# Performance work log

Measured on AMD Instinct MI355X. Metric: run time of the kernel, lower is better.

Reference implementation:

```python
import jax, jax.numpy as jnp
import numpy as np

L, H, D, FF = 4, 16, 1024, 4   # nLayers, nHeads, embedDim, ffMult
EPS = 1e-5


def layernorm(x, g, b):
    mu = jnp.mean(x, axis=-1, keepdims=True)
    var = jnp.mean(jnp.square(x - mu), axis=-1, keepdims=True)
    return (x - mu) * jax.lax.rsqrt(var + EPS) * g + b


def setup_inputs() -> dict:
    key = jax.random.key(0)
    ks = jax.random.split(key, 4)
    B, N = 2, 2048
    s = 0.02
    return {
        "x": jax.random.normal(ks[0], (B, N, D), jnp.float32),
        "Wqkv": jax.random.normal(ks[1], (L, D, 3 * D), jnp.float32) * s,
        "bqkv": jnp.zeros((L, 3 * D), jnp.float32),
        "W1": jax.random.normal(ks[2], (L, D, FF * D), jnp.float32) * s,
        "b1": jnp.zeros((L, FF * D), jnp.float32),
        "W2": jax.random.normal(ks[3], (L, FF * D, D), jnp.float32) * s,
        "b2": jnp.zeros((L, D), jnp.float32),
        "g1": jnp.ones((L, D), jnp.float32),
        "be1": jnp.zeros((L, D), jnp.float32),
        "g2": jnp.ones((L, D), jnp.float32),
        "be2": jnp.zeros((L, D), jnp.float32),
    }


def reference(x, Wqkv, bqkv, W1, b1, W2, b2, g1, be1, g2, be2):
    B, N, _ = x.shape
    dh = D // H
    scale = D ** -0.5  # NOTE: module scales by embedDim**-0.5, not head_dim
    act = lambda t: jax.nn.gelu(t, approximate=False)
    for l in range(L):
        qkv = x @ Wqkv[l] + bqkv[l]                       # [B,N,3D]
        q, k, v = jnp.split(qkv, 3, axis=-1)
        q = q.reshape(B, N, H, dh)
        k = k.reshape(B, N, H, dh)
        v = v.reshape(B, N, H, dh)
        scores = jnp.einsum('bihd,bjhd->bhij', q, k) * scale  # [B,H,N,N]
        z = jax.nn.softmax(scores, axis=-1)
        o = jnp.einsum('bhij,bjhd->bihd', z, v).reshape(B, N, D)
        h = layernorm(o + x, g1[l], be1[l])               # post-LN residual 1
        f = act(h @ W1[l] + b1[l])
        f = act(f @ W2[l] + b2[l])                        # activation after 2nd linear too (as in Sequential)
        x = layernorm(f + h, g2[l], be2[l])               # post-LN residual 2
    return x
```

## Files before the change

kernel.cpp:

```cpp
#include <hip/hip_runtime.h>
#include <hip/hip_bf16.h>
#include <cmath>


typedef __attribute__((ext_vector_type(8))) short bf16x8;
typedef __attribute__((ext_vector_type(4))) float f32x4;
typedef __hip_bfloat16 bf16;

#define DEV static __device__ __forceinline__

DEV unsigned short f2b(float f) {
    bf16 h = __float2bfloat16(f);
    return *reinterpret_cast<unsigned short*>(&h);
}

DEV unsigned int pack_bf16(float lo, float hi) {
    return (unsigned int)f2b(lo) | ((unsigned int)f2b(hi) << 16);
}

DEV float b2f(unsigned short u) {
    unsigned int x = ((unsigned int)u) << 16;
    return *reinterpret_cast<float*>(&x);
}

DEV float gelu_fast(float x) {
    float u = 0.7978845608028654f * fmaf(0.044715f * x, x * x, x);
    u = fminf(fmaxf(u, -15.f), 15.f);
    float t = __builtin_amdgcn_exp2f(u * 2.8853900817779268f);
    float th = (t - 1.0f) * __builtin_amdgcn_rcpf(t + 1.0f);
    return 0.5f * x * (1.0f + th);
}

DEV void gload_lds16(const bf16* g, bf16* l) {
    __builtin_amdgcn_global_load_lds(
        (const __attribute__((address_space(1))) void*)g,
        (__attribute__((address_space(3))) void*)l, 16, 0, 0);
}

__global__ __launch_bounds__(256) void transpose_cast(const float* __restrict__ W,
                                                      bf16* __restrict__ Wt,
                                                      int K, int Nm) {
    __shared__ float tile[32][33];
    const int l = blockIdx.z;
    const float* Wl = W + (size_t)l * K * Nm;
    bf16* Wtl = Wt + (size_t)l * K * Nm;
    const int n0 = blockIdx.x * 32, k0 = blockIdx.y * 32;
    const int tx = threadIdx.x, ty = threadIdx.y;
#pragma unroll
    for (int i = 0; i < 4; ++i)
        tile[ty + 8 * i][tx] = Wl[(size_t)(k0 + ty + 8 * i) * Nm + n0 + tx];
    __syncthreads();
#pragma unroll
    for (int i = 0; i < 4; ++i)
        Wtl[(size_t)(n0 + ty + 8 * i) * K + k0 + tx] = __float2bfloat16(tile[tx][ty + 8 * i]);
}

__global__ __launch_bounds__(256) void vtrans(const bf16* __restrict__ qkv,
                                              bf16* __restrict__ vtg, int N) {
    __shared__ bf16 tile[32][33];
    const int bh = blockIdx.z, b = bh >> 4, h = bh & 15;
    const int n0 = blockIdx.x * 32, d0 = blockIdx.y * 32;
    const int tx = threadIdx.x, ty = threadIdx.y;
    const bf16* src = qkv + (size_t)(b * N + n0) * 3072 + 2048 + h * 64 + d0;
#pragma unroll
    for (int i = 0; i < 4; ++i)
        tile[ty + 8 * i][tx] = src[(size_t)(ty + 8 * i) * 3072 + tx];
    __syncthreads();
    bf16* dst = vtg + ((size_t)bh * 64 + d0) * N + n0;
#pragma unroll
    for (int i = 0; i < 4; ++i)
        dst[(size_t)(ty + 8 * i) * N + tx] = tile[tx][ty + 8 * i];
}

__global__ __launch_bounds__(256) void cast_bf16_k(const float* __restrict__ in,
                                                   bf16* __restrict__ out, int n4) {
    int i = blockIdx.x * 256 + threadIdx.x;
    if (i >= n4) return;
    float4 v = reinterpret_cast<const float4*>(in)[i];
    ushort4 o = { f2b(v.x), f2b(v.y), f2b(v.z), f2b(v.w) };
    reinterpret_cast<ushort4*>(out)[i] = o;
}

template <int EPI>
__global__ __launch_bounds__(512, 2) void gemm256(const bf16* __restrict__ A,
                                                  const bf16* __restrict__ Bt,
                                                  const float* __restrict__ bias,
                                                  void* __restrict__ Cout,
                                                  int M, int Nm, int K,
                                                  int nbx, int ntiles, int Ktotal) {
    __shared__ bf16 As[2][256][64];
    __shared__ bf16 Bs[2][256][64];
    const int nwg = gridDim.x;
    int id = blockIdx.x;
    id = (id & 7) * (nwg >> 3) + (id >> 3);
    const int tile = id % ntiles, split = id / ntiles;
    const int m0 = (tile / nbx) * 256, n0 = (tile % nbx) * 256;
    const int kbase = split * K;
    const int t = threadIdx.x, w = t >> 6, lane = t & 63;
    const int wm = w >> 2, wn = w & 3;
    const int lr = lane & 15, lg = lane >> 4;
    const int srow = w * 8;
    const bf16* Ag = A + (size_t)(m0 + srow + (lane >> 3)) * Ktotal + kbase + (lane & 7) * 8;
    const bf16* Bg = Bt + (size_t)(n0 + srow + (lane >> 3)) * Ktotal + kbase + (lane & 7) * 8;

    f32x4 acc[8][4] = {};
    const int NT = K / 64;

#define STAGE256(kt, b)                                                          \
    {                                                                            \
        const size_t koff = (size_t)(kt) * 64;                                   \
        _Pragma("unroll")                                                        \
        for (int p = 0; p < 4; ++p)                                              \
            gload_lds16(Ag + (size_t)(p * 64) * Ktotal + koff,                   \
                        &As[b][p * 64 + srow][0]);                               \
        _Pragma("unroll")                                                        \
        for (int p = 0; p < 4; ++p)                                              \
            gload_lds16(Bg + (size_t)(p * 64) * Ktotal + koff,                   \
                        &Bs[b][p * 64 + srow][0]);                               \
    }

    STAGE256(0, 0);
    for (int kt = 0; kt < NT; ++kt) {
        const int buf = kt & 1;
        if (kt + 1 < NT) {
            STAGE256(kt + 1, buf ^ 1);
            asm volatile("s_waitcnt vmcnt(8)" ::: "memory");
        } else {
            asm volatile("s_waitcnt vmcnt(0)" ::: "memory");
        }
        __builtin_amdgcn_sched_barrier(0);
        __builtin_amdgcn_s_barrier();
        __builtin_amdgcn_sched_barrier(0);
        __builtin_amdgcn_s_setprio(1);
#pragma unroll
        for (int kk = 0; kk < 2; ++kk) {
            const int lk = kk * 32 + lg * 8;
            bf16x8 a[8], b[4];
#pragma unroll
            for (int m = 0; m < 8; ++m)
                a[m] = *reinterpret_cast<const bf16x8*>(&As[buf][wm * 128 + m * 16 + lr][lk]);
#pragma unroll
            for (int n = 0; n < 4; ++n)
                b[n] = *reinterpret_cast<const bf16x8*>(&Bs[buf][wn * 64 + n * 16 + lr][lk]);
#pragma unroll
            for (int m = 0; m < 8; ++m)
#pragma unroll
                for (int n = 0; n < 4; ++n)
                    acc[m][n] = __builtin_amdgcn_mfma_f32_16x16x32_bf16(a[m], b[n], acc[m][n], 0, 0, 0);
        }
        __builtin_amdgcn_s_setprio(0);
        __builtin_amdgcn_sched_barrier(0);
        __builtin_amdgcn_s_barrier();
        __builtin_amdgcn_sched_barrier(0);
    }
#undef STAGE256

    if (EPI == 3) {
        bf16* outp = (bf16*)Cout + (size_t)split * M * Nm;
#pragma unroll
        for (int n = 0; n < 4; ++n) {
            const int col = n0 + wn * 64 + n * 16 + lr;
#pragma unroll
            for (int m = 0; m < 8; ++m) {
                const int row = m0 + wm * 128 + m * 16 + lg * 4;
#pragma unroll
                for (int j = 0; j < 4; ++j)
                    outp[(size_t)(row + j) * Nm + col] = __float2bfloat16(acc[m][n][j]);
            }
        }
    } else {
#pragma unroll
        for (int n = 0; n < 4; ++n) {
            const int col = n0 + wn * 64 + n * 16 + lr;
            const float bc = bias[col];
#pragma unroll
            for (int m = 0; m < 8; ++m) {
                const int row = m0 + wm * 128 + m * 16 + lg * 4;
#pragma unroll
                for (int j = 0; j < 4; ++j) {
                    float v = acc[m][n][j] + bc;
                    if (EPI == 1) v = gelu_fast(v);
                    reinterpret_cast<bf16*>(Cout)[(size_t)(row + j) * Nm + col] = __float2bfloat16(v);
                }
            }
        }
    }
}

__global__ __launch_bounds__(256) void reduce4_gelu(const bf16* __restrict__ part,
                                                    const float* __restrict__ bias,
                                                    float* __restrict__ out,
                                                    int n8, int Nm8, size_t stride) {
    int i = blockIdx.x * 256 + threadIdx.x;
    if (i >= n8) return;
    const int cb = (i % Nm8) * 8;
    float s[8];
#pragma unroll
    for (int e = 0; e < 8; ++e) s[e] = bias[cb + e];
#pragma unroll
    for (int k = 0; k < 4; ++k) {
        bf16x8 v = *reinterpret_cast<const bf16x8*>(part + (size_t)k * stride + (size_t)i * 8);
#pragma unroll
        for (int e = 0; e < 8; ++e) s[e] += b2f((unsigned short)v[e]);
    }
    float4 r0 = { gelu_fast(s[0]), gelu_fast(s[1]), gelu_fast(s[2]), gelu_fast(s[3]) };
    float4 r1 = { gelu_fast(s[4]), gelu_fast(s[5]), gelu_fast(s[6]), gelu_fast(s[7]) };
    reinterpret_cast<float4*>(out)[2 * i]     = r0;
    reinterpret_cast<float4*>(out)[2 * i + 1] = r1;
}

__global__ __launch_bounds__(256) void attn_fwd(const bf16* __restrict__ qkv,
                                                const bf16* __restrict__ vtg,
                                                float* __restrict__ o, int N) {
    __shared__ bf16 Ks[2][64][72];
    __shared__ bf16 Vs[2][64][72];
    __shared__ bf16 Ps[4][32][72];
    const int nwg = gridDim.x, nbx = N / 128;
    int id = blockIdx.x;
    id = (id & 7) * (nwg >> 3) + (id >> 3);
    const int bh = id / nbx, b = bh >> 4, h = bh & 15;
    const int q0 = (id % nbx) * 128;
    const int t = threadIdx.x, w = t >> 6, lane = t & 63;
    const int lr = lane & 15, lg = lane >> 4;
    const bf16* base = qkv + (size_t)b * N * 3072;
    const bf16* vbase = vtg + (size_t)bh * 64 * N;

    bf16x8 qf[2][2];
#pragma unroll
    for (int rb = 0; rb < 2; ++rb) {
        const bf16* qp = base + (size_t)(q0 + w * 32 + rb * 16 + lr) * 3072 + h * 64 + lg * 8;
        qf[rb][0] = *reinterpret_cast<const bf16x8*>(qp);
        qf[rb][1] = *reinterpret_cast<const bf16x8*>(qp + 32);
    }

    float mrow[2] = { -INFINITY, -INFINITY };
    float lrow[2] = { 0.f, 0.f };
    f32x4 oacc[2][4] = {};
    const float scale2 = 0.03125f * 1.44269504088896340736f;
    const int srow = t >> 2, scolb = (t & 3) * 8;

    const bf16* kptr = base + (size_t)srow * 3072 + 1024 + h * 64 + scolb;
    const bf16* vptr = vbase + (size_t)srow * N + scolb;

    uint4 k0 = *reinterpret_cast<const uint4*>(kptr);
    uint4 k1 = *reinterpret_cast<const uint4*>(kptr + 32);
    uint4 v0 = *reinterpret_cast<const uint4*>(vptr);
    uint4 v1 = *reinterpret_cast<const uint4*>(vptr + 32);
    *reinterpret_cast<uint4*>(&Ks[0][srow][scolb])      = k0;
    *reinterpret_cast<uint4*>(&Ks[0][srow][scolb + 32]) = k1;
    *reinterpret_cast<uint4*>(&Vs[0][srow][scolb])      = v0;
    *reinterpret_cast<uint4*>(&Vs[0][srow][scolb + 32]) = v1;

    int cur = 0;
    for (int kv0 = 0; kv0 < N; kv0 += 64) {
        __syncthreads();
        const bool more = (kv0 + 64) < N;
        if (more) {
            const bf16* kn = kptr + (size_t)(kv0 + 64) * 3072;
            const bf16* vn = vptr + (kv0 + 64);
            k0 = *reinterpret_cast<const uint4*>(kn);
            k1 = *reinterpret_cast<const uint4*>(kn + 32);
            v0 = *reinterpret_cast<const uint4*>(vn);
            v1 = *reinterpret_cast<const uint4*>(vn + 32);
        }
        __builtin_amdgcn_sched_barrier(0);

        f32x4 st[2][4] = {};
#pragma unroll
        for (int f = 0; f < 2; ++f)
#pragma unroll
            for (int c = 0; c < 4; ++c) {
                bf16x8 ka = *reinterpret_cast<const bf16x8*>(&Ks[cur][c * 16 + lr][f * 32 + lg * 8]);
                st[0][c] = __builtin_amdgcn_mfma_f32_16x16x32_bf16(ka, qf[0][f], st[0][c], 0, 0, 0);
                st[1][c] = __builtin_amdgcn_mfma_f32_16x16x32_bf16(ka, qf[1][f], st[1][c], 0, 0, 0);
            }

#pragma unroll
        for (int rb = 0; rb < 2; ++rb) {
            float smax = st[rb][0][0];
#pragma unroll
            for (int c = 0; c < 4; ++c)
#pragma unroll
                for (int j = 0; j < 4; ++j) smax = fmaxf(smax, st[rb][c][j]);
            const float tilemax = smax * scale2;
            if (!__all(tilemax - mrow[rb] <= 11.0f)) {
                float tm = fmaxf(tilemax, __shfl_xor(tilemax, 16, 64));
                tm = fmaxf(tm, __shfl_xor(tm, 32, 64));
                const float mnew = fmaxf(mrow[rb], tm);
                const float al = __builtin_amdgcn_exp2f(mrow[rb] - mnew);
                mrow[rb] = mnew;
                lrow[rb] *= al;
#pragma unroll
                for (int c = 0; c < 4; ++c)
#pragma unroll
                    for (int j = 0; j < 4; ++j) oacc[rb][c][j] *= al;
            }
            float p[4][4];
            float psum = 0.f;
#pragma unroll
            for (int c = 0; c < 4; ++c)
#pragma unroll
                for (int j = 0; j < 4; ++j) {
                    p[c][j] = __builtin_amdgcn_exp2f(fmaf(st[rb][c][j], scale2, -mrow[rb]));
                    psum += p[c][j];
                }
            psum += __shfl_xor(psum, 16, 64);
            psum += __shfl_xor(psum, 32, 64);
            lrow[rb] += psum;
#pragma unroll
            for (int c = 0; c < 4; ++c) {
                uint2 pr = { pack_bf16(p[c][0], p[c][1]), pack_bf16(p[c][2], p[c][3]) };
                *reinterpret_cast<uint2*>(&Ps[w][rb * 16 + lr][c * 16 + lg * 4]) = pr;
            }
        }
        asm volatile("s_waitcnt lgkmcnt(0)" ::: "memory");
        __builtin_amdgcn_sched_barrier(0);

#pragma unroll
        for (int f = 0; f < 2; ++f) {
            bf16x8 pb0 = *reinterpret_cast<const bf16x8*>(&Ps[w][lr][f * 32 + lg * 8]);
            bf16x8 pb1 = *reinterpret_cast<const bf16x8*>(&Ps[w][16 + lr][f * 32 + lg * 8]);
#pragma unroll
            for (int c = 0; c < 4; ++c) {
                bf16x8 va = *reinterpret_cast<const bf16x8*>(&Vs[cur][c * 16 + lr][f * 32 + lg * 8]);
                oacc[0][c] = __builtin_amdgcn_mfma_f32_16x16x32_bf16(va, pb0, oacc[0][c], 0, 0, 0);
                oacc[1][c] = __builtin_amdgcn_mfma_f32_16x16x32_bf16(va, pb1, oacc[1][c], 0, 0, 0);
            }
        }

        if (more) {
            asm volatile("s_waitcnt vmcnt(0)" ::: "memory");
            __builtin_amdgcn_sched_barrier(0);
            *reinterpret_cast<uint4*>(&Ks[cur ^ 1][srow][scolb])      = k0;
            *reinterpret_cast<uint4*>(&Ks[cur ^ 1][srow][scolb + 32]) = k1;
            *reinterpret_cast<uint4*>(&Vs[cur ^ 1][srow][scolb])      = v0;
            *reinterpret_cast<uint4*>(&Vs[cur ^ 1][srow][scolb + 32]) = v1;
        }
        cur ^= 1;
    }

#pragma unroll
    for (int rb = 0; rb < 2; ++rb) {
        const float linv = 1.f / lrow[rb];
        float* op = o + ((size_t)b * N + q0 + w * 32 + rb * 16 + lr) * 1024 + h * 64;
#pragma unroll
        for (int c = 0; c < 4; ++c) {
            float4 v = { oacc[rb][c][0] * linv, oacc[rb][c][1] * linv,
                         oacc[rb][c][2] * linv, oacc[rb][c][3] * linv };
            *reinterpret_cast<float4*>(op + c * 16 + lg * 4) = v;
        }
    }
}

__global__ __launch_bounds__(256) void ln_res(const float* __restrict__ a,
                                              const float* __restrict__ r,
                                              const float* __restrict__ g,
                                              const float* __restrict__ be,
                                              float* __restrict__ y,
                                              bf16* __restrict__ yb) {
    const int row = blockIdx.x, t = threadIdx.x;
    float4 va = reinterpret_cast<const float4*>(a + (size_t)row * 1024)[t];
    float4 vr = reinterpret_cast<const float4*>(r + (size_t)row * 1024)[t];
    float v0 = va.x + vr.x, v1 = va.y + vr.y, v2 = va.z + vr.z, v3 = va.w + vr.w;
    float s1 = v0 + v1 + v2 + v3;
    float s2 = v0 * v0 + v1 * v1 + v2 * v2 + v3 * v3;
#pragma unroll
    for (int m = 1; m < 64; m <<= 1) {
        s1 += __shfl_xor(s1, m, 64);
        s2 += __shfl_xor(s2, m, 64);
    }
    __shared__ float ws1[4], ws2[4];
    if ((t & 63) == 0) { ws1[t >> 6] = s1; ws2[t >> 6] = s2; }
    __syncthreads();
    s1 = ws1[0] + ws1[1] + ws1[2] + ws1[3];
    s2 = ws2[0] + ws2[1] + ws2[2] + ws2[3];
    const float mean = s1 * (1.f / 1024.f);
    const float var = s2 * (1.f / 1024.f) - mean * mean;
    const float rstd = rsqrtf(var + 1e-5f);
    float4 gg = reinterpret_cast<const float4*>(g)[t];
    float4 bb = reinterpret_cast<const float4*>(be)[t];
    float o0 = (v0 - mean) * rstd * gg.x + bb.x;
    float o1 = (v1 - mean) * rstd * gg.y + bb.y;
    float o2 = (v2 - mean) * rstd * gg.z + bb.z;
    float o3 = (v3 - mean) * rstd * gg.w + bb.w;
    float4 out = { o0, o1, o2, o3 };
    reinterpret_cast<float4*>(y + (size_t)row * 1024)[t] = out;
    if (yb) {
        ushort4 ob = { f2b(o0), f2b(o1), f2b(o2), f2b(o3) };
        reinterpret_cast<ushort4*>(yb + (size_t)row * 1024)[t] = ob;
    }
}

extern "C" void kernel_launch(void* const* d_in, const int* in_sizes, int n_in,
                              void* d_out, int out_size, void* d_ws, size_t ws_size,
                              hipStream_t stream) {
    const float* x_in = (const float*)d_in[0];
    const float* Wqkv = (const float*)d_in[1];
    const float* bqkv = (const float*)d_in[2];
    const float* W1   = (const float*)d_in[3];
    const float* b1   = (const float*)d_in[4];
    const float* W2   = (const float*)d_in[5];
    const float* b2   = (const float*)d_in[6];
    const float* g1   = (const float*)d_in[7];
    const float* be1  = (const float*)d_in[8];
    const float* g2   = (const float*)d_in[9];
    const float* be2  = (const float*)d_in[10];

    const int Bv = 2, N = 2048, L = 4, Hh = 16;
    const int R = Bv * N;

    char* p = (char*)d_ws;
    auto alloc = [&](size_t bytes) { char* r = p; p += (bytes + 255) & ~(size_t)255; return r; };
    bf16*  Wqkvt = (bf16*)alloc((size_t)L * 3072 * 1024 * 2);
    bf16*  W1t   = (bf16*)alloc((size_t)L * 4096 * 1024 * 2);
    bf16*  W2t   = (bf16*)alloc((size_t)L * 1024 * 4096 * 2);
    bf16*  xb    = (bf16*)alloc((size_t)R * 1024 * 2);
    bf16*  qkvb  = (bf16*)alloc((size_t)R * 3072 * 2);
    float* obuf  = (float*)alloc((size_t)R * 1024 * 4);
    float* hbuf  = (float*)alloc((size_t)R * 1024 * 4);
    bf16*  hb    = (bf16*)alloc((size_t)R * 1024 * 2);
    bf16*  f1b   = (bf16*)alloc((size_t)R * 4096 * 2);
    float* xcur  = (float*)alloc((size_t)R * 1024 * 4);
    float* f2buf = obuf;
    bf16*  vtg   = (bf16*)hbuf;
    bf16*  part  = xb;

    transpose_cast<<<dim3(3072 / 32, 1024 / 32, L), dim3(32, 8), 0, stream>>>(Wqkv, Wqkvt, 1024, 3072);
    transpose_cast<<<dim3(4096 / 32, 1024 / 32, L), dim3(32, 8), 0, stream>>>(W1, W1t, 1024, 4096);
    transpose_cast<<<dim3(1024 / 32, 4096 / 32, L), dim3(32, 8), 0, stream>>>(W2, W2t, 4096, 1024);
    cast_bf16_k<<<(R * 1024 / 4 + 255) / 256, 256, 0, stream>>>(x_in, xb, R * 1024 / 4);

    const float* xres = x_in;
    for (int l = 0; l < L; ++l) {
        gemm256<0><<<(R / 256) * (3072 / 256), 512, 0, stream>>>(
            xb, Wqkvt + (size_t)l * 3072 * 1024, bqkv + l * 3072, qkvb,
            R, 3072, 1024, 3072 / 256, (R / 256) * (3072 / 256), 1024);
        vtrans<<<dim3(N / 32, 2, Bv * Hh), dim3(32, 8), 0, stream>>>(qkvb, vtg, N);
        attn_fwd<<<(N / 128) * (Bv * Hh), 256, 0, stream>>>(qkvb, vtg, obuf, N);
        ln_res<<<R, 256, 0, stream>>>(obuf, xres, g1 + l * 1024, be1 + l * 1024, hbuf, hb);
        gemm256<1><<<(R / 256) * (4096 / 256), 512, 0, stream>>>(
            hb, W1t + (size_t)l * 4096 * 1024, b1 + l * 4096, f1b,
            R, 4096, 1024, 4096 / 256, (R / 256) * (4096 / 256), 1024);
        gemm256<3><<<(R / 256) * (1024 / 256) * 4, 512, 0, stream>>>(
            f1b, W2t + (size_t)l * 1024 * 4096, nullptr, part,
            R, 1024, 1024, 1024 / 256, (R / 256) * (1024 / 256), 4096);
        reduce4_gelu<<<(R * 1024 / 8 + 255) / 256, 256, 0, stream>>>(
            part, b2 + l * 1024, f2buf, R * 1024 / 8, 1024 / 8, (size_t)R * 1024);
        float* xn = (l == L - 1) ? (float*)d_out : xcur;
        ln_res<<<R, 256, 0, stream>>>(f2buf, hbuf, g2 + l * 1024, be2 + l * 1024, xn, xb);
        xres = xn;
    }
}
```

Before: 1.098 ms.

## Fuse V transpose into QKV GEMM epilogue and split-K reduce into LayerNorm

The QKV GEMM epilogue now writes the V columns directly in transposed per-head layout, which removes the separate vtrans kernel. The split-K partial sums for the second FFN GEMM go to two aliased buffers (obuf and the now-dead qkvb). A new ln_res_red4 kernel sums the partials, adds bias, applies GELU and the residual, then does the LayerNorm. This drops the reduce4_gelu kernel and the fp32 round trip through f2buf. The cost is strided 8-byte transposed stores in the GEMM epilogue and more buffer aliasing that depends on kernel ordering.

Result: faster. 1.063 ms (-3.2%).

```diff
diff --git a/kernel.cpp b/kernel.cpp
--- a/kernel.cpp
+++ b/kernel.cpp
@@ -55,23 +55,6 @@
         Wtl[(size_t)(n0 + ty + 8 * i) * K + k0 + tx] = __float2bfloat16(tile[tx][ty + 8 * i]);
 }
 
-__global__ __launch_bounds__(256) void vtrans(const bf16* __restrict__ qkv,
-                                              bf16* __restrict__ vtg, int N) {
-    __shared__ bf16 tile[32][33];
-    const int bh = blockIdx.z, b = bh >> 4, h = bh & 15;
-    const int n0 = blockIdx.x * 32, d0 = blockIdx.y * 32;
-    const int tx = threadIdx.x, ty = threadIdx.y;
-    const bf16* src = qkv + (size_t)(b * N + n0) * 3072 + 2048 + h * 64 + d0;
-#pragma unroll
-    for (int i = 0; i < 4; ++i)
-        tile[ty + 8 * i][tx] = src[(size_t)(ty + 8 * i) * 3072 + tx];
-    __syncthreads();
-    bf16* dst = vtg + ((size_t)bh * 64 + d0) * N + n0;
-#pragma unroll
-    for (int i = 0; i < 4; ++i)
-        dst[(size_t)(ty + 8 * i) * N + tx] = tile[tx][ty + 8 * i];
-}
-
 __global__ __launch_bounds__(256) void cast_bf16_k(const float* __restrict__ in,
                                                    bf16* __restrict__ out, int n4) {
     int i = blockIdx.x * 256 + threadIdx.x;
@@ -86,6 +69,7 @@
                                                   const bf16* __restrict__ Bt,
                                                   const float* __restrict__ bias,
                                                   void* __restrict__ Cout,
+                                                  void* __restrict__ Cout2,
                                                   int M, int Nm, int K,
                                                   int nbx, int ntiles, int Ktotal) {
     __shared__ bf16 As[2][256][64];
@@ -156,7 +140,9 @@
 #undef STAGE256
 
     if (EPI == 3) {
-        bf16* outp = (bf16*)Cout + (size_t)split * M * Nm;
+        bf16* outp = (split < 2)
+            ? (bf16*)Cout + (size_t)split * M * Nm
+            : (bf16*)Cout2 + (size_t)(split - 2) * M * Nm;
 #pragma unroll
         for (int n = 0; n < 4; ++n) {
             const int col = n0 + wn * 64 + n * 16 + lr;
@@ -166,6 +152,22 @@
 #pragma unroll
                 for (int j = 0; j < 4; ++j)
                     outp[(size_t)(row + j) * Nm + col] = __float2bfloat16(acc[m][n][j]);
+            }
+        }
+    } else if (EPI == 4 && n0 >= 2048) {
+#pragma unroll
+        for (int n = 0; n < 4; ++n) {
+            const int col = n0 + wn * 64 + n * 16 + lr;
+            const float bc = bias[col];
+            const int vcol = col - 2048;
+#pragma unroll
+            for (int m = 0; m < 8; ++m) {
+                const int row = m0 + wm * 128 + m * 16 + lg * 4;
+                const int b = row >> 11, nn = row & 2047;
+                ushort4 o = { f2b(acc[m][n][0] + bc), f2b(acc[m][n][1] + bc),
+                              f2b(acc[m][n][2] + bc), f2b(acc[m][n][3] + bc) };
+                *reinterpret_cast<ushort4*>(
+                    (bf16*)Cout2 + ((size_t)(b * 1024 + vcol)) * 2048 + nn) = o;
             }
         }
     } else {
@@ -185,28 +187,6 @@
             }
         }
     }
-}
-
-__global__ __launch_bounds__(256) void reduce4_gelu(const bf16* __restrict__ part,
-                                                    const float* __restrict__ bias,
-                                                    float* __restrict__ out,
-                                                    int n8, int Nm8, size_t stride) {
-    int i = blockIdx.x * 256 + threadIdx.x;
-    if (i >= n8) return;
-    const int cb = (i % Nm8) * 8;
-    float s[8];
-#pragma unroll
-    for (int e = 0; e < 8; ++e) s[e] = bias[cb + e];
-#pragma unroll
-    for (int k = 0; k < 4; ++k) {
-        bf16x8 v = *reinterpret_cast<const bf16x8*>(part + (size_t)k * stride + (size_t)i * 8);
-#pragma unroll
-        for (int e = 0; e < 8; ++e) s[e] += b2f((unsigned short)v[e]);
-    }
-    float4 r0 = { gelu_fast(s[0]), gelu_fast(s[1]), gelu_fast(s[2]), gelu_fast(s[3]) };
-    float4 r1 = { gelu_fast(s[4]), gelu_fast(s[5]), gelu_fast(s[6]), gelu_fast(s[7]) };
-    reinterpret_cast<float4*>(out)[2 * i]     = r0;
-    reinterpret_cast<float4*>(out)[2 * i + 1] = r1;
 }
 
 __global__ __launch_bounds__(256) void attn_fwd(const bf16* __restrict__ qkv,
@@ -391,6 +371,58 @@
     }
 }
 
+__global__ __launch_bounds__(256) void ln_res_red4(const bf16* __restrict__ p0,
+                                                   const bf16* __restrict__ p2,
+                                                   const float* __restrict__ bias,
+                                                   const float* __restrict__ r,
+                                                   const float* __restrict__ g,
+                                                   const float* __restrict__ be,
+                                                   float* __restrict__ y,
+                                                   bf16* __restrict__ yb,
+                                                   size_t stride) {
+    const int row = blockIdx.x, t = threadIdx.x;
+    const size_t off = (size_t)row * 1024 + t * 4;
+    float4 bb4 = reinterpret_cast<const float4*>(bias)[t];
+    float s0 = bb4.x, s1v = bb4.y, s2v = bb4.z, s3 = bb4.w;
+#pragma unroll
+    for (int k = 0; k < 2; ++k) {
+        ushort4 va = *reinterpret_cast<const ushort4*>(p0 + k * stride + off);
+        s0 += b2f(va.x); s1v += b2f(va.y); s2v += b2f(va.z); s3 += b2f(va.w);
+        ushort4 vb = *reinterpret_cast<const ushort4*>(p2 + k * stride + off);
+        s0 += b2f(vb.x); s1v += b2f(vb.y); s2v += b2f(vb.z); s3 += b2f(vb.w);
+    }
+    float4 vr = reinterpret_cast<const float4*>(r + (size_t)row * 1024)[t];
+    float v0 = gelu_fast(s0) + vr.x;
+    float v1 = gelu_fast(s1v) + vr.y;
+    float v2 = gelu_fast(s2v) + vr.z;
+    float v3 = gelu_fast(s3) + vr.w;
+    float s1 = v0 + v1 + v2 + v3;
+    float s2 = v0 * v0 + v1 * v1 + v2 * v2 + v3 * v3;
+#pragma unroll
+    for (int m = 1; m < 64; m <<= 1) {
+        s1 += __shfl_xor(s1, m, 64);
+        s2 += __shfl_xor(s2, m, 64);
+    }
+    __shared__ float ws1[4], ws2[4];
+    if ((t & 63) == 0) { ws1[t >> 6] = s1; ws2[t >> 6] = s2; }
+    __syncthreads();
+    s1 = ws1[0] + ws1[1] + ws1[2] + ws1[3];
+    s2 = ws2[0] + ws2[1] + ws2[2] + ws2[3];
+    const float mean = s1 * (1.f / 1024.f);
+    const float var = s2 * (1.f / 1024.f) - mean * mean;
+    const float rstd = rsqrtf(var + 1e-5f);
+    float4 gg = reinterpret_cast<const float4*>(g)[t];
+    float4 bb = reinterpret_cast<const float4*>(be)[t];
+    float o0 = (v0 - mean) * rstd * gg.x + bb.x;
+    float o1 = (v1 - mean) * rstd * gg.y + bb.y;
+    float o2 = (v2 - mean) * rstd * gg.z + bb.z;
+    float o3 = (v3 - mean) * rstd * gg.w + bb.w;
+    float4 out = { o0, o1, o2, o3 };
+    reinterpret_cast<float4*>(y + (size_t)row * 1024)[t] = out;
+    ushort4 ob = { f2b(o0), f2b(o1), f2b(o2), f2b(o3) };
+    reinterpret_cast<ushort4*>(yb + (size_t)row * 1024)[t] = ob;
+}
+
 extern "C" void kernel_launch(void* const* d_in, const int* in_sizes, int n_in,
                               void* d_out, int out_size, void* d_ws, size_t ws_size,
                               hipStream_t stream) {
@@ -421,9 +453,9 @@
     bf16*  hb    = (bf16*)alloc((size_t)R * 1024 * 2);
     bf16*  f1b   = (bf16*)alloc((size_t)R * 4096 * 2);
     float* xcur  = (float*)alloc((size_t)R * 1024 * 4);
-    float* f2buf = obuf;
     bf16*  vtg   = (bf16*)hbuf;
-    bf16*  part  = xb;
+    bf16*  part0 = (bf16*)obuf;
+    bf16*  part2 = (bf16*)qkvb;
 
     transpose_cast<<<dim3(3072 / 32, 1024 / 32, L), dim3(32, 8), 0, stream>>>(Wqkv, Wqkvt, 1024, 3072);
     transpose_cast<<<dim3(4096 / 32, 1024 / 32, L), dim3(32, 8), 0, stream>>>(W1, W1t, 1024, 4096);
@@ -432,22 +464,21 @@
 
     const float* xres = x_in;
     for (int l = 0; l < L; ++l) {
-        gemm256<0><<<(R / 256) * (3072 / 256), 512, 0, stream>>>(
-            xb, Wqkvt + (size_t)l * 3072 * 1024, bqkv + l * 3072, qkvb,
+        gemm256<4><<<(R / 256) * (3072 / 256), 512, 0, stream>>>(
+            xb, Wqkvt + (size_t)l * 3072 * 1024, bqkv + l * 3072, qkvb, vtg,
             R, 3072, 1024, 3072 / 256, (R / 256) * (3072 / 256), 1024);
-        vtrans<<<dim3(N / 32, 2, Bv * Hh), dim3(32, 8), 0, stream>>>(qkvb, vtg, N);
         attn_fwd<<<(N / 128) * (Bv * Hh), 256, 0, stream>>>(qkvb, vtg, obuf, N);
         ln_res<<<R, 256, 0, stream>>>(obuf, xres, g1 + l * 1024, be1 + l * 1024, hbuf, hb);
         gemm256<1><<<(R / 256) * (4096 / 256), 512, 0, stream>>>(
-            hb, W1t + (size_t)l * 4096 * 1024, b1 + l * 4096, f1b,
+            hb, W1t + (size_t)l * 4096 * 1024, b1 + l * 4096, f1b, nullptr,
             R, 4096, 1024, 4096 / 256, (R / 256) * (4096 / 256), 1024);
         gemm256<3><<<(R / 256) * (1024 / 256) * 4, 512, 0, stream>>>(
-            f1b, W2t + (size_t)l * 1024 * 4096, nullptr, part,
+            f1b, W2t + (size_t)l * 1024 * 4096, nullptr, part0, part2,
             R, 1024, 1024, 1024 / 256, (R / 256) * (1024 / 256), 4096);
-        reduce4_gelu<<<(R * 1024 / 8 + 255) / 256, 256, 0, stream>>>(
-            part, b2 + l * 1024, f2buf, R * 1024 / 8, 1024 / 8, (size_t)R * 1024);
         float* xn = (l == L - 1) ? (float*)d_out : xcur;
-        ln_res<<<R, 256, 0, stream>>>(f2buf, hbuf, g2 + l * 1024, be2 + l * 1024, xn, xb);
+        ln_res_red4<<<R, 256, 0, stream>>>(part0, part2, b2 + l * 1024, hbuf,
+                                           g2 + l * 1024, be2 + l * 1024, xn, xb,
+                                           (size_t)R * 1024);
         xres = xn;
     }
 }
```
